# Optimization experiments

Hardware: AMD Instinct MI355X
Metric: run time of the kernel (lower is better)

## Reference

```python
import jax, jax.numpy as jnp
import numpy as np

HEADS, DHEAD = 8, 32
INNER = HEADS * DHEAD  # 256


def _conv3x3(x, w, b):
    y = jax.lax.conv_general_dilated(x, w, (1, 1), ((1, 1), (1, 1)),
                                     dimension_numbers=('NCHW', 'OIHW', 'NCHW'))
    return y + b[None, :, None, None]


def _conv1x1(x, w, b):
    return jnp.einsum('oc,bchw->bohw', w, x) + b[None, :, None, None]


def setup_inputs() -> dict:
    key = jax.random.key(0)
    ks = jax.random.split(key, 16)
    s = 0.02
    return {
        'x': jax.random.normal(ks[0], (2, 256, 48, 48), jnp.float32),
        'luma': jax.random.uniform(ks[1], (2, 1, 48, 48), jnp.float32),
        'w_qkv': jax.random.normal(ks[2], (768, 256), jnp.float32) * s,
        'b_qkv': jax.random.normal(ks[3], (768,), jnp.float32) * s,
        'w_proj': jax.random.normal(ks[4], (256, 256), jnp.float32) * s,
        'b_proj': jax.random.normal(ks[5], (256,), jnp.float32) * s,
        'w_c1': jax.random.normal(ks[6], (128, 1, 3, 3), jnp.float32) * s,
        'b_c1': jax.random.normal(ks[7], (128,), jnp.float32) * s,
        'w_c2': jax.random.normal(ks[8], (128, 128, 3, 3), jnp.float32) * s,
        'b_c2': jax.random.normal(ks[9], (128,), jnp.float32) * s,
        'w_g': jax.random.normal(ks[10], (256, 128), jnp.float32) * s,
        'b_g': jax.random.normal(ks[11], (256,), jnp.float32) * s,
        'w_bt': jax.random.normal(ks[12], (256, 128), jnp.float32) * s,
        'b_bt': jax.random.normal(ks[13], (256,), jnp.float32) * s,
        'alpha': jax.random.normal(ks[14], (), jnp.float32) * 0.1,
    }


def reference(x, luma, w_qkv, b_qkv, w_proj, b_proj, w_c1, b_c1, w_c2, b_c2,
              w_g, b_g, w_bt, b_bt, alpha):
    B, C, H, W = x.shape
    N = H * W
    scale = DHEAD ** -0.5

    def to_heads(t):  # [B, h*d, H, W] -> [B, h, N, d]
        return t.reshape(B, HEADS, DHEAD, N).transpose(0, 1, 3, 2)

    qkv = _conv1x1(x, w_qkv, b_qkv)
    q = to_heads(qkv[:, 0 * INNER:1 * INNER])
    k = to_heads(qkv[:, 1 * INNER:2 * INNER])
    v = to_heads(qkv[:, 2 * INNER:3 * INNER])

    # luma conditioning net
    h = jax.nn.relu(_conv3x3(luma, w_c1, b_c1))
    h = jax.nn.relu(_conv3x3(h, w_c2, b_c2))
    gamma = to_heads(_conv1x1(h, w_g, b_g))
    beta = to_heads(_conv1x1(h, w_bt, b_bt))
    q = gamma * q + beta
    k = gamma * k + beta
    v = gamma * v + beta

    # luminance bias: avg_pool2d(3, stride=1, pad=1, count_include_pad=True)
    invL = 1.0 - luma
    invL = jax.lax.reduce_window(invL, 0.0, jax.lax.add, (1, 1, 3, 3), (1, 1, 1, 1),
                                 ((0, 0), (0, 0), (1, 1), (1, 1))) / 9.0
    invL = invL.reshape(B, N)
    invL = invL - invL.mean(axis=-1, keepdims=True)
    q = q + alpha * invL[:, None, :, None]

    attn = jax.nn.softmax(jnp.einsum('bhid,bhjd->bhij', q, k) * scale, axis=-1)
    out = jnp.einsum('bhij,bhjd->bhid', attn, v)
    out = out.transpose(0, 1, 3, 2).reshape(B, INNER, H, W)
    return _conv1x1(out, w_proj, b_proj)
```

## Files before the change

kernel.cpp:

```cpp
#include <hip/hip_runtime.h>
#include <hip/hip_bf16.h>
#include <math.h>
#include <string.h>

#define NB 2
#define NN 2304
#define NHEADS 8
#define DH 32
#define AW 8
#define KPW 288

typedef __attribute__((ext_vector_type(8))) short v8s;
typedef __attribute__((ext_vector_type(4))) float v4f;

__device__ inline unsigned short f2b(float f) {
    unsigned u = __builtin_bit_cast(unsigned, f);
    unsigned r = u + 0x7FFFu + ((u >> 16) & 1u);
    return (unsigned short)(r >> 16);
}
__device__ inline float b2f(short s) {
    unsigned u = ((unsigned)(unsigned short)s) << 16;
    return __builtin_bit_cast(float, u);
}
__device__ inline unsigned pk2(float a, float b) {
    __hip_bfloat162 h = __float22bfloat162_rn(make_float2(a, b));
    unsigned r;
    memcpy(&r, &h, sizeof(r));
    return r;
}
__device__ inline float blo(unsigned u) { return __builtin_bit_cast(float, u << 16); }
__device__ inline float bhi(unsigned u) { return __builtin_bit_cast(float, u & 0xffff0000u); }

__global__ void k_front(const float* __restrict__ x, short* __restrict__ xt,
                        const float* __restrict__ luma, float* __restrict__ invl,
                        const float* __restrict__ wc1, const float* __restrict__ bc1,
                        short* __restrict__ h1p,
                        const float* __restrict__ wc2, const float* __restrict__ wqkv,
                        const float* __restrict__ wg, const float* __restrict__ wbt,
                        const float* __restrict__ wproj,
                        short* __restrict__ tc2b, short* __restrict__ wqkvb,
                        short* __restrict__ wgb, short* __restrict__ wbtb,
                        short* __restrict__ wprojb, float* __restrict__ vsum) {
    __shared__ unsigned short lds[64 * 66];
    __shared__ float red[256];
    int blk = blockIdx.x;
    const int XT_END = NB * 144;
    const int INVL_END = XT_END + NB;
    const int CONV1_END = INVL_END + NB * 1250;
    if (blk >= CONV1_END) {
        int i = (blk - CONV1_END) * 256 + threadIdx.x;
        if (i < 16 * DH) vsum[i] = 0.f;
        if (i < 9 * 128 * 128) {
            int s = i / (128 * 128);
            int rem = i % (128 * 128);
            int o = rem / 128, ic = rem % 128;
            tc2b[i] = (short)f2b(wc2[(o * 128 + ic) * 9 + s]);
        }
        if (i < 768 * 256) wqkvb[i] = (short)f2b(wqkv[i]);
        if (i < 256 * 128) { wgb[i] = (short)f2b(wg[i]); wbtb[i] = (short)f2b(wbt[i]); }
        if (i < 256 * 256) wprojb[i] = (short)f2b(wproj[i]);
        return;
    }
    if (blk >= INVL_END) {
        int cb = blk - INVL_END;
        int c = threadIdx.x & 127;
        int p = (cb % 1250) * 2 + (threadIdx.x >> 7);
        int b = cb / 1250;
        int py = p / 50, px = p % 50;
        float val = 0.f;
        if (py >= 1 && py <= 48 && px >= 1 && px <= 48) {
            int y = py - 1, xx0 = px - 1;
            const float* lb = luma + b * NN;
            float acc = bc1[c];
#pragma unroll
            for (int ky = 0; ky < 3; ++ky) {
                int yy = y + ky - 1;
                if (yy < 0 || yy >= 48) continue;
#pragma unroll
                for (int kx = 0; kx < 3; ++kx) {
                    int xx = xx0 + kx - 1;
                    if (xx < 0 || xx >= 48) continue;
                    acc += wc1[c * 9 + ky * 3 + kx] * lb[yy * 48 + xx];
                }
            }
            val = fmaxf(acc, 0.f);
        }
        h1p[((size_t)b * 2500 + p) * 128 + c] = (short)f2b(val);
        return;
    }
    if (blk >= XT_END) {
        int b = blk - XT_END;
        const float* lb = luma + b * NN;
        float pooled[9];
        float local = 0.f;
#pragma unroll
        for (int it = 0; it < 9; ++it) {
            int n = it * 256 + threadIdx.x;
            int y = n / 48, xx0 = n % 48;
            float s = 0.f;
            for (int ky = 0; ky < 3; ++ky) {
                int yy = y + ky - 1;
                if (yy < 0 || yy >= 48) continue;
                for (int kx = 0; kx < 3; ++kx) {
                    int xx = xx0 + kx - 1;
                    if (xx < 0 || xx >= 48) continue;
                    s += 1.f - lb[yy * 48 + xx];
                }
            }
            s *= (1.f / 9.f);
            pooled[it] = s;
            local += s;
        }
        red[threadIdx.x] = local;
        __syncthreads();
        for (int off = 128; off > 0; off >>= 1) {
            if (threadIdx.x < off) red[threadIdx.x] += red[threadIdx.x + off];
            __syncthreads();
        }
        float mean = red[0] * (1.f / NN);
#pragma unroll
        for (int it = 0; it < 9; ++it) {
            int n = it * 256 + threadIdx.x;
            invl[b * NN + n] = pooled[it] - mean;
        }
        return;
    }
    int nt = blk % 36, ct = (blk / 36) % 4, b = blk / 144;
    int n0 = nt * 64, c0 = ct * 64;
    int nc = threadIdx.x & 63, cr = threadIdx.x >> 6;
#pragma unroll
    for (int i = 0; i < 16; ++i) {
        int cs = i * 4 + cr;
        float v = x[((size_t)b * 256 + c0 + cs) * NN + n0 + nc];
        lds[nc * 66 + cs] = f2b(v);
    }
    __syncthreads();
    int cc = threadIdx.x & 31, nr = threadIdx.x >> 5;
    unsigned* xt2 = (unsigned*)xt;
#pragma unroll
    for (int j = 0; j < 8; ++j) {
        int ns = j * 8 + nr;
        unsigned w = *(unsigned*)&lds[ns * 66 + 2 * cc];
        xt2[(((size_t)b * NN + n0 + ns) * 256 + c0) / 2 + cc] = w;
    }
}

__global__ __launch_bounds__(64) void k_conv2m(const short* __restrict__ h1p,
                                               const short* __restrict__ tc2b,
                                               const float* __restrict__ bc2,
                                               short* __restrict__ h2t) {
    int lane = threadIdx.x, l15 = lane & 15, g = lane >> 4;
    int blk = blockIdx.x;
    int ntg = blk % 36, ot = (blk / 36) % 8, b = blk / (36 * 8);
    int p0[4], na[4];
#pragma unroll
    for (int j = 0; j < 4; ++j) {
        int nt = ntg * 4 + j;
        int y = nt / 3, xx = (nt % 3) * 16;
        p0[j] = (y + 1) * 50 + xx + 1;
        na[j] = y * 48 + xx + l15;
    }
    const short* hb = h1p + (size_t)b * 2500 * 128;

    v4f acc[4] = {{0.f,0.f,0.f,0.f},{0.f,0.f,0.f,0.f},{0.f,0.f,0.f,0.f},{0.f,0.f,0.f,0.f}};
#pragma unroll
    for (int s = 0; s < 9; ++s) {
        int dp = (s / 3 - 1) * 50 + (s % 3 - 1);
#pragma unroll
        for (int kk = 0; kk < 4; ++kk) {
            v8s A = *(const v8s*)(tc2b + ((size_t)(s * 128 + ot * 16 + l15)) * 128 + kk * 32 + 8 * g);
#pragma unroll
            for (int j = 0; j < 4; ++j) {
                v8s B = *(const v8s*)(hb + (size_t)(p0[j] + dp + l15) * 128 + kk * 32 + 8 * g);
                acc[j] = __builtin_amdgcn_mfma_f32_16x16x32_bf16(A, B, acc[j], 0, 0, 0);
            }
        }
    }
    v4f bias = *(const v4f*)&bc2[ot * 16 + 4 * g];
#pragma unroll
    for (int j = 0; j < 4; ++j) {
        uint2 w;
        w.x = pk2(fmaxf(acc[j][0] + bias[0], 0.f), fmaxf(acc[j][1] + bias[1], 0.f));
        w.y = pk2(fmaxf(acc[j][2] + bias[2], 0.f), fmaxf(acc[j][3] + bias[3], 0.f));
        *(uint2*)&h2t[((size_t)b * NN + na[j]) * 128 + ot * 16 + 4 * g] = w;
    }
}

__global__ __launch_bounds__(64) void k_gbm(const short* __restrict__ h2t,
                                            const short* __restrict__ wgb,
                                            const short* __restrict__ wbtb,
                                            const float* __restrict__ bg,
                                            const float* __restrict__ bbt,
                                            short* __restrict__ gtb, short* __restrict__ bttb) {
    int lane = threadIdx.x, l15 = lane & 15, g = lane >> 4;
    int blk = blockIdx.x;
    int ntg = blk % 36, ot = (blk / 36) % 16, b = blk / (36 * 16);
    int n0 = ntg * 64;
    const short* hb = h2t + (size_t)b * NN * 128;

    v4f ga[4] = {{0.f,0.f,0.f,0.f},{0.f,0.f,0.f,0.f},{0.f,0.f,0.f,0.f},{0.f,0.f,0.f,0.f}};
    v4f ta[4] = {{0.f,0.f,0.f,0.f},{0.f,0.f,0.f,0.f},{0.f,0.f,0.f,0.f},{0.f,0.f,0.f,0.f}};
#pragma unroll
    for (int kk = 0; kk < 4; ++kk) {
        v8s Ag = *(const v8s*)(wgb + (size_t)(ot * 16 + l15) * 128 + kk * 32 + 8 * g);
        v8s At = *(const v8s*)(wbtb + (size_t)(ot * 16 + l15) * 128 + kk * 32 + 8 * g);
#pragma unroll
        for (int j = 0; j < 4; ++j) {
            v8s B = *(const v8s*)(hb + (size_t)(n0 + j * 16 + l15) * 128 + kk * 32 + 8 * g);
            ga[j] = __builtin_amdgcn_mfma_f32_16x16x32_bf16(Ag, B, ga[j], 0, 0, 0);
            ta[j] = __builtin_amdgcn_mfma_f32_16x16x32_bf16(At, B, ta[j], 0, 0, 0);
        }
    }
    v4f bgv = *(const v4f*)&bg[ot * 16 + 4 * g];
    v4f bbv = *(const v4f*)&bbt[ot * 16 + 4 * g];
#pragma unroll
    for (int j = 0; j < 4; ++j) {
        size_t o = ((size_t)b * NN + n0 + j * 16 + l15) * 256 + ot * 16 + 4 * g;
        uint2 w;
        w.x = pk2(ga[j][0] + bgv[0], ga[j][1] + bgv[1]);
        w.y = pk2(ga[j][2] + bgv[2], ga[j][3] + bgv[3]);
        *(uint2*)&gtb[o] = w;
        w.x = pk2(ta[j][0] + bbv[0], ta[j][1] + bbv[1]);
        w.y = pk2(ta[j][2] + bbv[2], ta[j][3] + bbv[3]);
        *(uint2*)&bttb[o] = w;
    }
}

__global__ __launch_bounds__(64) void k_qkvm(const short* __restrict__ xt,
                                             const short* __restrict__ wqkvb,
                                             const float* __restrict__ bqkv,
                                             const short* __restrict__ gtb,
                                             const short* __restrict__ bttb,
                                             const float* __restrict__ invl,
                                             const float* __restrict__ alpha_p,
                                             short* __restrict__ qb, short* __restrict__ kb,
                                             short* __restrict__ vraw) {
    int lane = threadIdx.x, l15 = lane & 15, g = lane >> 4;
    int blk = blockIdx.x;
    int ntg = blk % 36, otg = (blk / 36) % 24, b = blk / (36 * 24);
    int n0 = ntg * 64;
    const short* xb = xt + (size_t)b * NN * 256;

    v4f acc[2][4];
#pragma unroll
    for (int oa = 0; oa < 2; ++oa)
#pragma unroll
        for (int j = 0; j < 4; ++j) acc[oa][j] = (v4f){0.f, 0.f, 0.f, 0.f};
#pragma unroll
    for (int kk = 0; kk < 8; ++kk) {
        v8s A0 = *(const v8s*)(wqkvb + (size_t)(otg * 32 + l15) * 256 + kk * 32 + 8 * g);
        v8s A1 = *(const v8s*)(wqkvb + (size_t)(otg * 32 + 16 + l15) * 256 + kk * 32 + 8 * g);
#pragma unroll
        for (int j = 0; j < 4; ++j) {
            v8s B = *(const v8s*)(xb + (size_t)(n0 + j * 16 + l15) * 256 + kk * 32 + 8 * g);
            acc[0][j] = __builtin_amdgcn_mfma_f32_16x16x32_bf16(A0, B, acc[0][j], 0, 0, 0);
            acc[1][j] = __builtin_amdgcn_mfma_f32_16x16x32_bf16(A1, B, acc[1][j], 0, 0, 0);
        }
    }
    const float scale = 0.25503486f;
    float alpha = *alpha_p;
#pragma unroll
    for (int oa = 0; oa < 2; ++oa) {
        int ocb = otg * 32 + oa * 16;
        int which = ocb >> 8;
        int cbase = (ocb & 255) + 4 * g;
        int h = cbase >> 5, dbase = cbase & 31;
        v4f bias = *(const v4f*)&bqkv[ocb + 4 * g];
        short* dst = (which == 0) ? qb : (which == 1) ? kb : vraw;
#pragma unroll
        for (int j = 0; j < 4; ++j) {
            int n = n0 + j * 16 + l15;
            v4f a = acc[oa][j];
            uint2 gg = *(const uint2*)&gtb[((size_t)b * NN + n) * 256 + cbase];
            uint2 tt = *(const uint2*)&bttb[((size_t)b * NN + n) * 256 + cbase];
            float iv = (which == 0) ? alpha * invl[b * NN + n] : 0.f;
            float v0 = blo(gg.x) * (a[0] + bias[0]) + blo(tt.x);
            float v1 = bhi(gg.x) * (a[1] + bias[1]) + bhi(tt.x);
            float v2 = blo(gg.y) * (a[2] + bias[2]) + blo(tt.y);
            float v3 = bhi(gg.y) * (a[3] + bias[3]) + bhi(tt.y);
            if (which == 0) {
                v0 = (v0 + iv) * scale; v1 = (v1 + iv) * scale;
                v2 = (v2 + iv) * scale; v3 = (v3 + iv) * scale;
            }
            uint2 w;
            w.x = pk2(v0, v1);
            w.y = pk2(v2, v3);
            *(uint2*)&dst[(((size_t)b * NHEADS + h) * NN + n) * DH + dbase] = w;
        }
    }
}

__global__ void k_vt(const short* __restrict__ vraw, short* __restrict__ vtb,
                     float* __restrict__ vsum) {
    __shared__ unsigned short lds[64 * 34];
    int bh = blockIdx.x / 36, nc = blockIdx.x % 36;
    int n0 = nc * 64;
    int dpair = threadIdx.x & 15, nsub = (threadIdx.x >> 4) & 15;
    const unsigned* vr2 = (const unsigned*)vraw;
#pragma unroll
    for (int i = 0; i < 4; ++i) {
        int ns = i * 16 + nsub;
        unsigned v = vr2[((size_t)bh * NN + n0 + ns) * 16 + dpair];
        *(unsigned*)&lds[ns * 34 + 2 * dpair] = v;
    }
    __syncthreads();
    int pn = threadIdx.x & 31, drow = threadIdx.x >> 5;
    int kb0 = n0 >> 5;
    unsigned* vtb2 = (unsigned*)vtb;
#pragma unroll
    for (int j = 0; j < 4; ++j) {
        int d = j * 8 + drow;
        unsigned lo = lds[(2 * pn) * 34 + d];
        unsigned hi = lds[(2 * pn + 1) * 34 + d];
        vtb2[(((size_t)bh * 72 + kb0 + (pn >> 4)) * 32 + d) * 16 + (pn & 15)] = lo | (hi << 16);
    }
    if (threadIdx.x < 32) {
        int d = threadIdx.x;
        float s = 0.f;
        for (int ns = 0; ns < 64; ++ns) s += b2f((short)lds[ns * 34 + d]);
        atomicAdd(&vsum[bh * DH + d], s);
    }
}

__global__ __launch_bounds__(512) void k_attn2(const short* __restrict__ qb,
                                               const short* __restrict__ kbuf,
                                               const short* __restrict__ vtb,
                                               const float* __restrict__ vsum,
                                               short* __restrict__ aotb) {
    __shared__ short plds[AW][64 * 40];
    __shared__ short acch[AW][64][36];
    __shared__ float ps_lds[AW][64];
    int tid = threadIdx.x;
    int w = tid >> 6, lane = tid & 63;
    int l15 = lane & 15, g = lane >> 4;
    int blk = blockIdx.x;
    int logical = (blk & 7) * 72 + (blk >> 3);
    int qt = logical % 36, bh = logical / 36;
    int qbase = qt * 64;

    const short* qp = qb + ((size_t)bh * NN + qbase) * DH;
    const short* kp = kbuf + ((size_t)bh * NN + w * KPW) * DH;
    const short* vp = vtb + ((size_t)bh * 72 + w * (KPW / 32)) * 1024;

    v8s q0 = *(const v8s*)(qp + l15 * DH + 8 * g);
    v8s q1 = *(const v8s*)(qp + (16 + l15) * DH + 8 * g);
    v8s q2 = *(const v8s*)(qp + (32 + l15) * DH + 8 * g);
    v8s q3 = *(const v8s*)(qp + (48 + l15) * DH + 8 * g);

    const short one_b = (short)0x3F80;
    const v8s ones = {one_b, one_b, one_b, one_b, one_b, one_b, one_b, one_b};

    v4f acc[2][4];
#pragma unroll
    for (int dt = 0; dt < 2; ++dt)
#pragma unroll
        for (int qf = 0; qf < 4; ++qf) acc[dt][qf] = (v4f){0.f, 0.f, 0.f, 0.f};
    v4f ps[4] = {{0.f,0.f,0.f,0.f},{0.f,0.f,0.f,0.f},{0.f,0.f,0.f,0.f},{0.f,0.f,0.f,0.f}};
    short* pw = plds[w];

    for (int it = 0; it < KPW / 32; ++it) {
        const short* kpi = kp + it * 32 * DH;
        v8s ka0 = *(const v8s*)(kpi + l15 * DH + 8 * g);
        v8s ka1 = *(const v8s*)(kpi + (16 + l15) * DH + 8 * g);
        v4f s00 = __builtin_amdgcn_mfma_f32_16x16x32_bf16(ka0, q0, (v4f){0.f,0.f,0.f,0.f}, 0, 0, 0);
        v4f s01 = __builtin_amdgcn_mfma_f32_16x16x32_bf16(ka0, q1, (v4f){0.f,0.f,0.f,0.f}, 0, 0, 0);
        v4f s02 = __builtin_amdgcn_mfma_f32_16x16x32_bf16(ka0, q2, (v4f){0.f,0.f,0.f,0.f}, 0, 0, 0);
        v4f s03 = __builtin_amdgcn_mfma_f32_16x16x32_bf16(ka0, q3, (v4f){0.f,0.f,0.f,0.f}, 0, 0, 0);
        v4f s10 = __builtin_amdgcn_mfma_f32_16x16x32_bf16(ka1, q0, (v4f){0.f,0.f,0.f,0.f}, 0, 0, 0);
        v4f s11 = __builtin_amdgcn_mfma_f32_16x16x32_bf16(ka1, q1, (v4f){0.f,0.f,0.f,0.f}, 0, 0, 0);
        v4f s12 = __builtin_amdgcn_mfma_f32_16x16x32_bf16(ka1, q2, (v4f){0.f,0.f,0.f,0.f}, 0, 0, 0);
        v4f s13 = __builtin_amdgcn_mfma_f32_16x16x32_bf16(ka1, q3, (v4f){0.f,0.f,0.f,0.f}, 0, 0, 0);

#define DOFRAG(S, QF, KT)                                                        \
        {                                                                        \
            float p0 = __builtin_amdgcn_exp2f((S)[0]) - 1.f;                     \
            float p1 = __builtin_amdgcn_exp2f((S)[1]) - 1.f;                     \
            float p2 = __builtin_amdgcn_exp2f((S)[2]) - 1.f;                     \
            float p3 = __builtin_amdgcn_exp2f((S)[3]) - 1.f;                     \
            uint2 wv;                                                            \
            wv.x = pk2(p0, p1);                                                  \
            wv.y = pk2(p2, p3);                                                  \
            *(uint2*)((char*)pw + ((QF) * 16 + l15) * 80 + ((KT) * 16 + 4 * g) * 2) = wv; \
        }
        DOFRAG(s00, 0, 0)
        DOFRAG(s01, 1, 0)
        DOFRAG(s02, 2, 0)
        DOFRAG(s03, 3, 0)
        DOFRAG(s10, 0, 1)
        DOFRAG(s11, 1, 1)
        DOFRAG(s12, 2, 1)
        DOFRAG(s13, 3, 1)
#undef DOFRAG
        v8s pa0 = *(v8s*)((char*)pw + l15 * 80 + 16 * g);
        v8s pa1 = *(v8s*)((char*)pw + (16 + l15) * 80 + 16 * g);
        v8s pa2 = *(v8s*)((char*)pw + (32 + l15) * 80 + 16 * g);
        v8s pa3 = *(v8s*)((char*)pw + (48 + l15) * 80 + 16 * g);
        const short* vpi = vp + it * 1024;
        v8s vb0 = *(const v8s*)(vpi + l15 * 32 + 8 * g);
        v8s vb1 = *(const v8s*)(vpi + (16 + l15) * 32 + 8 * g);
        __builtin_amdgcn_s_setprio(1);
        acc[0][0] = __builtin_amdgcn_mfma_f32_16x16x32_bf16(pa0, vb0, acc[0][0], 0, 0, 0);
        acc[1][0] = __builtin_amdgcn_mfma_f32_16x16x32_bf16(pa0, vb1, acc[1][0], 0, 0, 0);
        acc[0][1] = __builtin_amdgcn_mfma_f32_16x16x32_bf16(pa1, vb0, acc[0][1], 0, 0, 0);
        acc[1][1] = __builtin_amdgcn_mfma_f32_16x16x32_bf16(pa1, vb1, acc[1][1], 0, 0, 0);
        acc[0][2] = __builtin_amdgcn_mfma_f32_16x16x32_bf16(pa2, vb0, acc[0][2], 0, 0, 0);
        acc[1][2] = __builtin_amdgcn_mfma_f32_16x16x32_bf16(pa2, vb1, acc[1][2], 0, 0, 0);
        acc[0][3] = __builtin_amdgcn_mfma_f32_16x16x32_bf16(pa3, vb0, acc[0][3], 0, 0, 0);
        acc[1][3] = __builtin_amdgcn_mfma_f32_16x16x32_bf16(pa3, vb1, acc[1][3], 0, 0, 0);
        ps[0] = __builtin_amdgcn_mfma_f32_16x16x32_bf16(pa0, ones, ps[0], 0, 0, 0);
        ps[1] = __builtin_amdgcn_mfma_f32_16x16x32_bf16(pa1, ones, ps[1], 0, 0, 0);
        ps[2] = __builtin_amdgcn_mfma_f32_16x16x32_bf16(pa2, ones, ps[2], 0, 0, 0);
        ps[3] = __builtin_amdgcn_mfma_f32_16x16x32_bf16(pa3, ones, ps[3], 0, 0, 0);
        __builtin_amdgcn_s_setprio(0);
    }

    if (l15 == 0) {
#pragma unroll
        for (int qf = 0; qf < 4; ++qf)
#pragma unroll
            for (int r = 0; r < 4; ++r)
                ps_lds[w][qf * 16 + 4 * g + r] = ps[qf][r];
    }
#pragma unroll
    for (int qf = 0; qf < 4; ++qf)
#pragma unroll
        for (int r = 0; r < 4; ++r) {
            acch[w][qf * 16 + 4 * g + r][l15]      = (short)f2b(acc[0][qf][r]);
            acch[w][qf * 16 + 4 * g + r][16 + l15] = (short)f2b(acc[1][qf][r]);
        }
    __syncthreads();

    int q = tid >> 3, d0 = (tid & 7) * 4;
    float L = (float)NN;
    float a0 = 0.f, a1 = 0.f, a2 = 0.f, a3 = 0.f;
#pragma unroll
    for (int wv = 0; wv < AW; ++wv) {
        L += ps_lds[wv][q];
        const short* row = &acch[wv][q][d0];
        a0 += b2f(row[0]); a1 += b2f(row[1]); a2 += b2f(row[2]); a3 += b2f(row[3]);
    }
    const float* vs = vsum + bh * DH + d0;
    float rl = 1.f / L;
    uint2 o;
    o.x = pk2((a0 + vs[0]) * rl, (a1 + vs[1]) * rl);
    o.y = pk2((a2 + vs[2]) * rl, (a3 + vs[3]) * rl);
    int b = bh >> 3, h = bh & 7;
    *(uint2*)&aotb[((size_t)b * NN + qbase + q) * 256 + h * DH + d0] = o;
}

__global__ __launch_bounds__(64) void k_projm(const short* __restrict__ aotb,
                                              const short* __restrict__ wprojb,
                                              const float* __restrict__ bproj,
                                              float* __restrict__ out) {
    int lane = threadIdx.x, l15 = lane & 15, g = lane >> 4;
    int blk = blockIdx.x;
    int ntg = blk % 36, otg = (blk / 36) % 8, b = blk / (36 * 8);
    int n0 = ntg * 64;
    const short* ab = aotb + (size_t)b * NN * 256;

    v4f acc[2][4];
#pragma unroll
    for (int oa = 0; oa < 2; ++oa)
#pragma unroll
        for (int j = 0; j < 4; ++j) acc[oa][j] = (v4f){0.f, 0.f, 0.f, 0.f};
#pragma unroll
    for (int kk = 0; kk < 8; ++kk) {
        v8s A0 = *(const v8s*)(wprojb + (size_t)(otg * 32 + l15) * 256 + kk * 32 + 8 * g);
        v8s A1 = *(const v8s*)(wprojb + (size_t)(otg * 32 + 16 + l15) * 256 + kk * 32 + 8 * g);
#pragma unroll
        for (int j = 0; j < 4; ++j) {
            v8s B = *(const v8s*)(ab + (size_t)(n0 + j * 16 + l15) * 256 + kk * 32 + 8 * g);
            acc[0][j] = __builtin_amdgcn_mfma_f32_16x16x32_bf16(A0, B, acc[0][j], 0, 0, 0);
            acc[1][j] = __builtin_amdgcn_mfma_f32_16x16x32_bf16(A1, B, acc[1][j], 0, 0, 0);
        }
    }
#pragma unroll
    for (int oa = 0; oa < 2; ++oa) {
        v4f bias = *(const v4f*)&bproj[otg * 32 + oa * 16 + 4 * g];
#pragma unroll
        for (int j = 0; j < 4; ++j) {
#pragma unroll
            for (int r = 0; r < 4; ++r) {
                int o = otg * 32 + oa * 16 + 4 * g + r;
                out[((size_t)b * 256 + o) * NN + n0 + j * 16 + l15] = acc[oa][j][r] + bias[r];
            }
        }
    }
}

extern "C" void kernel_launch(void* const* d_in, const int* in_sizes, int n_in,
                              void* d_out, int out_size, void* d_ws, size_t ws_size,
                              hipStream_t stream) {
    const float* x     = (const float*)d_in[0];
    const float* luma  = (const float*)d_in[1];
    const float* wqkv  = (const float*)d_in[2];
    const float* bqkv  = (const float*)d_in[3];
    const float* wproj = (const float*)d_in[4];
    const float* bproj = (const float*)d_in[5];
    const float* wc1   = (const float*)d_in[6];
    const float* bc1   = (const float*)d_in[7];
    const float* wc2   = (const float*)d_in[8];
    const float* bc2   = (const float*)d_in[9];
    const float* wg    = (const float*)d_in[10];
    const float* bg    = (const float*)d_in[11];
    const float* wbt   = (const float*)d_in[12];
    const float* bbt   = (const float*)d_in[13];
    const float* alpha = (const float*)d_in[14];
    float* out = (float*)d_out;

    float* ws = (float*)d_ws;
    size_t off = 0;
    short* tc2b = (short*)(ws + off);  off += 9 * 128 * 128 / 2;
    short* wqkvb = (short*)(ws + off); off += 768 * 256 / 2;
    short* wgb = (short*)(ws + off);   off += 256 * 128 / 2;
    short* wbtb = (short*)(ws + off);  off += 256 * 128 / 2;
    short* wprojb = (short*)(ws + off); off += 256 * 256 / 2;
    short* h1p = (short*)(ws + off);   off += NB * 2500 * 128 / 2;
    short* xt = (short*)(ws + off);    off += NB * NN * 256 / 2;
    short* h2t = (short*)(ws + off);   off += NB * NN * 128 / 2;
    short* gtb = (short*)(ws + off);   off += NB * NN * 256 / 2;
    short* bttb = (short*)(ws + off);  off += NB * NN * 256 / 2;
    float* invl = ws + off;            off += NB * NN;
    short* qbb = (short*)(ws + off);   off += 16 * NN * DH / 2;
    short* kbb = (short*)(ws + off);   off += 16 * NN * DH / 2;
    short* vraw = (short*)(ws + off);  off += 16 * NN * DH / 2;
    short* vtb = (short*)(ws + off);   off += 16 * NN * DH / 2;
    float* vsum = ws + off;            off += 16 * DH;
    short* aotb = (short*)(ws + off);  off += NB * NN * 256 / 2;
    (void)ws_size; (void)in_sizes; (void)n_in; (void)out_size;

    int front_grid = NB * 144 + NB + NB * 1250 + 768;
    k_front<<<front_grid, 256, 0, stream>>>(x, xt, luma, invl, wc1, bc1, h1p,
                                            wc2, wqkv, wg, wbt, wproj,
                                            tc2b, wqkvb, wgb, wbtb, wprojb, vsum);
    k_conv2m<<<NB * 8 * 36, 64, 0, stream>>>(h1p, tc2b, bc2, h2t);
    k_gbm<<<NB * 16 * 36, 64, 0, stream>>>(h2t, wgb, wbtb, bg, bbt, gtb, bttb);
    k_qkvm<<<NB * 24 * 36, 64, 0, stream>>>(xt, wqkvb, bqkv, gtb, bttb, invl, alpha,
                                            qbb, kbb, vraw);
    k_vt<<<16 * 36, 256, 0, stream>>>(vraw, vtb, vsum);
    k_attn2<<<576, 512, 0, stream>>>(qbb, kbb, vtb, vsum, aotb);
    k_projm<<<NB * 8 * 36, 64, 0, stream>>>(aotb, wprojb, bproj, out);
}
```

Before: 98.71 us.

## Fuse conv2 with gamma/beta projection and fold V transpose into QKV kernel

Merges the 3x3 conv2 kernel and the gamma/beta 1x1 projection into one kernel. Each block computes a 16-pixel tile of all 128 conv2 channels into LDS and then projects it to gamma and beta, so the h2t intermediate buffer is no longer written and read back. The V transpose and per-head V sum move into the QKV kernel's epilogue through LDS, which removes the vraw buffer and the k_vt launch. This saves two launches and the intermediate global traffic, but the fused conv kernel runs only 288 blocks of 256 threads, so parallelism may be lower than before.

```diff
diff --git a/kernel.cpp b/kernel.cpp
--- a/kernel.cpp
+++ b/kernel.cpp
@@ -145,84 +145,74 @@
     }
 }
 
-__global__ __launch_bounds__(64) void k_conv2m(const short* __restrict__ h1p,
-                                               const short* __restrict__ tc2b,
-                                               const float* __restrict__ bc2,
-                                               short* __restrict__ h2t) {
-    int lane = threadIdx.x, l15 = lane & 15, g = lane >> 4;
+__global__ __launch_bounds__(256) void k_cgb(const short* __restrict__ h1p,
+                                             const short* __restrict__ tc2b,
+                                             const float* __restrict__ bc2,
+                                             const short* __restrict__ wgb,
+                                             const short* __restrict__ wbtb,
+                                             const float* __restrict__ bg,
+                                             const float* __restrict__ bbt,
+                                             short* __restrict__ gtb,
+                                             short* __restrict__ bttb) {
+    __shared__ unsigned short h2l[16][136];
+    int tid = threadIdx.x;
+    int w = tid >> 6, lane = tid & 63;
+    int l15 = lane & 15, g = lane >> 4;
     int blk = blockIdx.x;
-    int ntg = blk % 36, ot = (blk / 36) % 8, b = blk / (36 * 8);
-    int p0[4], na[4];
-#pragma unroll
-    for (int j = 0; j < 4; ++j) {
-        int nt = ntg * 4 + j;
-        int y = nt / 3, xx = (nt % 3) * 16;
-        p0[j] = (y + 1) * 50 + xx + 1;
-        na[j] = y * 48 + xx + l15;
-    }
+    int nt = blk % 144, b = blk / 144;
+    int y = nt / 3, x0 = (nt % 3) * 16;
+    int n0 = y * 48 + x0;
+    int p0 = (y + 1) * 50 + x0 + 1;
     const short* hb = h1p + (size_t)b * 2500 * 128;
 
-    v4f acc[4] = {{0.f,0.f,0.f,0.f},{0.f,0.f,0.f,0.f},{0.f,0.f,0.f,0.f},{0.f,0.f,0.f,0.f}};
+    v4f acc0 = {0.f,0.f,0.f,0.f}, acc1 = acc0;
 #pragma unroll
     for (int s = 0; s < 9; ++s) {
         int dp = (s / 3 - 1) * 50 + (s % 3 - 1);
 #pragma unroll
         for (int kk = 0; kk < 4; ++kk) {
-            v8s A = *(const v8s*)(tc2b + ((size_t)(s * 128 + ot * 16 + l15)) * 128 + kk * 32 + 8 * g);
-#pragma unroll
-            for (int j = 0; j < 4; ++j) {
-                v8s B = *(const v8s*)(hb + (size_t)(p0[j] + dp + l15) * 128 + kk * 32 + 8 * g);
-                acc[j] = __builtin_amdgcn_mfma_f32_16x16x32_bf16(A, B, acc[j], 0, 0, 0);
-            }
-        }
-    }
-    v4f bias = *(const v4f*)&bc2[ot * 16 + 4 * g];
-#pragma unroll
-    for (int j = 0; j < 4; ++j) {
-        uint2 w;
-        w.x = pk2(fmaxf(acc[j][0] + bias[0], 0.f), fmaxf(acc[j][1] + bias[1], 0.f));
-        w.y = pk2(fmaxf(acc[j][2] + bias[2], 0.f), fmaxf(acc[j][3] + bias[3], 0.f));
-        *(uint2*)&h2t[((size_t)b * NN + na[j]) * 128 + ot * 16 + 4 * g] = w;
-    }
-}
-
-__global__ __launch_bounds__(64) void k_gbm(const short* __restrict__ h2t,
-                                            const short* __restrict__ wgb,
-                                            const short* __restrict__ wbtb,
-                                            const float* __restrict__ bg,
-                                            const float* __restrict__ bbt,
-                                            short* __restrict__ gtb, short* __restrict__ bttb) {
-    int lane = threadIdx.x, l15 = lane & 15, g = lane >> 4;
-    int blk = blockIdx.x;
-    int ntg = blk % 36, ot = (blk / 36) % 16, b = blk / (36 * 16);
-    int n0 = ntg * 64;
-    const short* hb = h2t + (size_t)b * NN * 128;
-
-    v4f ga[4] = {{0.f,0.f,0.f,0.f},{0.f,0.f,0.f,0.f},{0.f,0.f,0.f,0.f},{0.f,0.f,0.f,0.f}};
-    v4f ta[4] = {{0.f,0.f,0.f,0.f},{0.f,0.f,0.f,0.f},{0.f,0.f,0.f,0.f},{0.f,0.f,0.f,0.f}};
-#pragma unroll
-    for (int kk = 0; kk < 4; ++kk) {
-        v8s Ag = *(const v8s*)(wgb + (size_t)(ot * 16 + l15) * 128 + kk * 32 + 8 * g);
-        v8s At = *(const v8s*)(wbtb + (size_t)(ot * 16 + l15) * 128 + kk * 32 + 8 * g);
-#pragma unroll
-        for (int j = 0; j < 4; ++j) {
-            v8s B = *(const v8s*)(hb + (size_t)(n0 + j * 16 + l15) * 128 + kk * 32 + 8 * g);
-            ga[j] = __builtin_amdgcn_mfma_f32_16x16x32_bf16(Ag, B, ga[j], 0, 0, 0);
-            ta[j] = __builtin_amdgcn_mfma_f32_16x16x32_bf16(At, B, ta[j], 0, 0, 0);
-        }
-    }
-    v4f bgv = *(const v4f*)&bg[ot * 16 + 4 * g];
-    v4f bbv = *(const v4f*)&bbt[ot * 16 + 4 * g];
-#pragma unroll
-    for (int j = 0; j < 4; ++j) {
-        size_t o = ((size_t)b * NN + n0 + j * 16 + l15) * 256 + ot * 16 + 4 * g;
-        uint2 w;
-        w.x = pk2(ga[j][0] + bgv[0], ga[j][1] + bgv[1]);
-        w.y = pk2(ga[j][2] + bgv[2], ga[j][3] + bgv[3]);
-        *(uint2*)&gtb[o] = w;
-        w.x = pk2(ta[j][0] + bbv[0], ta[j][1] + bbv[1]);
-        w.y = pk2(ta[j][2] + bbv[2], ta[j][3] + bbv[3]);
-        *(uint2*)&bttb[o] = w;
+            v8s B = *(const v8s*)(hb + (size_t)(p0 + dp + l15) * 128 + kk * 32 + 8 * g);
+            v8s A0 = *(const v8s*)(tc2b + ((size_t)(s * 128 + (2 * w) * 16 + l15)) * 128 + kk * 32 + 8 * g);
+            v8s A1 = *(const v8s*)(tc2b + ((size_t)(s * 128 + (2 * w + 1) * 16 + l15)) * 128 + kk * 32 + 8 * g);
+            acc0 = __builtin_amdgcn_mfma_f32_16x16x32_bf16(A0, B, acc0, 0, 0, 0);
+            acc1 = __builtin_amdgcn_mfma_f32_16x16x32_bf16(A1, B, acc1, 0, 0, 0);
+        }
+    }
+    {
+        v4f bias0 = *(const v4f*)&bc2[(2 * w) * 16 + 4 * g];
+        v4f bias1 = *(const v4f*)&bc2[(2 * w + 1) * 16 + 4 * g];
+        uint2 wv;
+        wv.x = pk2(fmaxf(acc0[0] + bias0[0], 0.f), fmaxf(acc0[1] + bias0[1], 0.f));
+        wv.y = pk2(fmaxf(acc0[2] + bias0[2], 0.f), fmaxf(acc0[3] + bias0[3], 0.f));
+        *(uint2*)&h2l[l15][(2 * w) * 16 + 4 * g] = wv;
+        wv.x = pk2(fmaxf(acc1[0] + bias1[0], 0.f), fmaxf(acc1[1] + bias1[1], 0.f));
+        wv.y = pk2(fmaxf(acc1[2] + bias1[2], 0.f), fmaxf(acc1[3] + bias1[3], 0.f));
+        *(uint2*)&h2l[l15][(2 * w + 1) * 16 + 4 * g] = wv;
+    }
+    __syncthreads();
+
+#pragma unroll
+    for (int idx = 0; idx < 4; ++idx) {
+        int ot = w + idx * 4;
+        v4f ga = {0.f,0.f,0.f,0.f}, ta = ga;
+#pragma unroll
+        for (int kk = 0; kk < 4; ++kk) {
+            v8s B = *(const v8s*)&h2l[l15][kk * 32 + 8 * g];
+            v8s Ag = *(const v8s*)(wgb + (size_t)(ot * 16 + l15) * 128 + kk * 32 + 8 * g);
+            v8s At = *(const v8s*)(wbtb + (size_t)(ot * 16 + l15) * 128 + kk * 32 + 8 * g);
+            ga = __builtin_amdgcn_mfma_f32_16x16x32_bf16(Ag, B, ga, 0, 0, 0);
+            ta = __builtin_amdgcn_mfma_f32_16x16x32_bf16(At, B, ta, 0, 0, 0);
+        }
+        v4f bgv = *(const v4f*)&bg[ot * 16 + 4 * g];
+        v4f bbv = *(const v4f*)&bbt[ot * 16 + 4 * g];
+        size_t o = ((size_t)b * NN + n0 + l15) * 256 + ot * 16 + 4 * g;
+        uint2 wv;
+        wv.x = pk2(ga[0] + bgv[0], ga[1] + bgv[1]);
+        wv.y = pk2(ga[2] + bgv[2], ga[3] + bgv[3]);
+        *(uint2*)&gtb[o] = wv;
+        wv.x = pk2(ta[0] + bbv[0], ta[1] + bbv[1]);
+        wv.y = pk2(ta[2] + bbv[2], ta[3] + bbv[3]);
+        *(uint2*)&bttb[o] = wv;
     }
 }
 
@@ -234,7 +224,8 @@
                                              const float* __restrict__ invl,
                                              const float* __restrict__ alpha_p,
                                              short* __restrict__ qb, short* __restrict__ kb,
-                                             short* __restrict__ vraw) {
+                                             short* __restrict__ vtb, float* __restrict__ vsum) {
+    __shared__ unsigned short vlds[64][36];
     int lane = threadIdx.x, l15 = lane & 15, g = lane >> 4;
     int blk = blockIdx.x;
     int ntg = blk % 36, otg = (blk / 36) % 24, b = blk / (36 * 24);
@@ -259,14 +250,14 @@
     }
     const float scale = 0.25503486f;
     float alpha = *alpha_p;
+    int which = (otg * 32) >> 8;
 #pragma unroll
     for (int oa = 0; oa < 2; ++oa) {
         int ocb = otg * 32 + oa * 16;
-        int which = ocb >> 8;
         int cbase = (ocb & 255) + 4 * g;
         int h = cbase >> 5, dbase = cbase & 31;
         v4f bias = *(const v4f*)&bqkv[ocb + 4 * g];
-        short* dst = (which == 0) ? qb : (which == 1) ? kb : vraw;
+        short* dst = (which == 0) ? qb : kb;
 #pragma unroll
         for (int j = 0; j < 4; ++j) {
             int n = n0 + j * 16 + l15;
@@ -282,43 +273,35 @@
                 v0 = (v0 + iv) * scale; v1 = (v1 + iv) * scale;
                 v2 = (v2 + iv) * scale; v3 = (v3 + iv) * scale;
             }
-            uint2 w;
-            w.x = pk2(v0, v1);
-            w.y = pk2(v2, v3);
-            *(uint2*)&dst[(((size_t)b * NHEADS + h) * NN + n) * DH + dbase] = w;
-        }
-    }
-}
-
-__global__ void k_vt(const short* __restrict__ vraw, short* __restrict__ vtb,
-                     float* __restrict__ vsum) {
-    __shared__ unsigned short lds[64 * 34];
-    int bh = blockIdx.x / 36, nc = blockIdx.x % 36;
-    int n0 = nc * 64;
-    int dpair = threadIdx.x & 15, nsub = (threadIdx.x >> 4) & 15;
-    const unsigned* vr2 = (const unsigned*)vraw;
-#pragma unroll
-    for (int i = 0; i < 4; ++i) {
-        int ns = i * 16 + nsub;
-        unsigned v = vr2[((size_t)bh * NN + n0 + ns) * 16 + dpair];
-        *(unsigned*)&lds[ns * 34 + 2 * dpair] = v;
-    }
-    __syncthreads();
-    int pn = threadIdx.x & 31, drow = threadIdx.x >> 5;
-    int kb0 = n0 >> 5;
-    unsigned* vtb2 = (unsigned*)vtb;
-#pragma unroll
-    for (int j = 0; j < 4; ++j) {
-        int d = j * 8 + drow;
-        unsigned lo = lds[(2 * pn) * 34 + d];
-        unsigned hi = lds[(2 * pn + 1) * 34 + d];
-        vtb2[(((size_t)bh * 72 + kb0 + (pn >> 4)) * 32 + d) * 16 + (pn & 15)] = lo | (hi << 16);
-    }
-    if (threadIdx.x < 32) {
-        int d = threadIdx.x;
-        float s = 0.f;
-        for (int ns = 0; ns < 64; ++ns) s += b2f((short)lds[ns * 34 + d]);
-        atomicAdd(&vsum[bh * DH + d], s);
+            uint2 wv;
+            wv.x = pk2(v0, v1);
+            wv.y = pk2(v2, v3);
+            if (which == 2) {
+                *(uint2*)&vlds[j * 16 + l15][oa * 16 + 4 * g] = wv;
+            } else {
+                *(uint2*)&dst[(((size_t)b * NHEADS + h) * NN + n) * DH + dbase] = wv;
+            }
+        }
+    }
+    if (which == 2) {
+        __syncthreads();
+        int bh = b * NHEADS + (otg - 16);
+        int kb0 = ntg * 2;
+        int kp = lane & 31, dh = lane >> 5;
+        unsigned* vtb2 = (unsigned*)vtb;
+#pragma unroll
+        for (int dd = 0; dd < 16; ++dd) {
+            int d = dh * 16 + dd;
+            unsigned lo = vlds[2 * kp][d];
+            unsigned hi = vlds[2 * kp + 1][d];
+            vtb2[(((size_t)bh * 72 + kb0 + (kp >> 4)) * 32 + d) * 16 + (kp & 15)] = lo | (hi << 16);
+        }
+        if (lane < 32) {
+            int d = lane;
+            float s = 0.f;
+            for (int ns = 0; ns < 64; ++ns) s += b2f((short)vlds[ns][d]);
+            atomicAdd(&vsum[bh * DH + d], s);
+        }
     }
 }
 
@@ -517,13 +500,11 @@
     short* wprojb = (short*)(ws + off); off += 256 * 256 / 2;
     short* h1p = (short*)(ws + off);   off += NB * 2500 * 128 / 2;
     short* xt = (short*)(ws + off);    off += NB * NN * 256 / 2;
-    short* h2t = (short*)(ws + off);   off += NB * NN * 128 / 2;
     short* gtb = (short*)(ws + off);   off += NB * NN * 256 / 2;
     short* bttb = (short*)(ws + off);  off += NB * NN * 256 / 2;
     float* invl = ws + off;            off += NB * NN;
     short* qbb = (short*)(ws + off);   off += 16 * NN * DH / 2;
     short* kbb = (short*)(ws + off);   off += 16 * NN * DH / 2;
-    short* vraw = (short*)(ws + off);  off += 16 * NN * DH / 2;
     short* vtb = (short*)(ws + off);   off += 16 * NN * DH / 2;
     float* vsum = ws + off;            off += 16 * DH;
     short* aotb = (short*)(ws + off);  off += NB * NN * 256 / 2;
@@ -533,11 +514,9 @@
     k_front<<<front_grid, 256, 0, stream>>>(x, xt, luma, invl, wc1, bc1, h1p,
                                             wc2, wqkv, wg, wbt, wproj,
                                             tc2b, wqkvb, wgb, wbtb, wprojb, vsum);
-    k_conv2m<<<NB * 8 * 36, 64, 0, stream>>>(h1p, tc2b, bc2, h2t);
-    k_gbm<<<NB * 16 * 36, 64, 0, stream>>>(h2t, wgb, wbtb, bg, bbt, gtb, bttb);
+    k_cgb<<<NB * 144, 256, 0, stream>>>(h1p, tc2b, bc2, wgb, wbtb, bg, bbt, gtb, bttb);
     k_qkvm<<<NB * 24 * 36, 64, 0, stream>>>(xt, wqkvb, bqkv, gtb, bttb, invl, alpha,
-                                            qbb, kbb, vraw);
-    k_vt<<<16 * 36, 256, 0, stream>>>(vraw, vtb, vsum);
+                                            qbb, kbb, vtb, vsum);
     k_attn2<<<576, 512, 0, stream>>>(qbb, kbb, vtb, vsum, aotb);
     k_projm<<<NB * 8 * 36, 64, 0, stream>>>(aotb, wprojb, bproj, out);
 }
```

Result: slower. 106.1 us (+7.5%).
